# Kernel optimization log

Hardware: AMD Instinct MI355X
Metric: run time of the kernel (lower is better)

## Reference

```python
import jax, jax.numpy as jnp
import numpy as np

B, N, F_IN, F_OUT = 4, 4096, 128, 128

def setup_inputs() -> dict:
    key = jax.random.key(0)
    k1, k2, k3 = jax.random.split(key, 3)
    x = jax.random.normal(k1, (B, N, F_IN), dtype=jnp.float32)
    adj = jax.random.uniform(k2, (B, N, N), dtype=jnp.float32)
    weight = jax.random.normal(k3, (F_IN, F_OUT), dtype=jnp.float32) * (6.0 / (F_IN + F_OUT)) ** 0.5
    bias = jnp.zeros((F_OUT,), dtype=jnp.float32)
    return {"x": x, "adj": adj, "weight": weight, "bias": bias}

def reference(x, adj, weight, bias):
    # Z = D^{-1/2} A D^{-1/2} X W + b   (activation=None)
    degree = jnp.sum(adj, axis=-1)                       # [B, N]
    d_inv = jnp.power(degree + 1e-6, -0.5)               # [B, N]
    # diag(d_inv) @ A @ diag(d_inv) == row/col elementwise scaling
    adj_norm = d_inv[:, :, None] * adj * d_inv[:, None, :]  # [B, N, N]
    z = jnp.einsum('bnm,bmf->bnf', adj_norm, x)          # [B, N, F_in]
    z = jnp.einsum('bnf,fo->bno', z, weight) + bias      # [B, N, F_out]
    return z
```

## Files before the change

### kernel.cpp

```cpp
#include <hip/hip_runtime.h>
#include <hip/hip_bf16.h>
#include <stdint.h>


#define NROW 4096
#define FDIM 128
#define NBATCH 4

typedef __bf16 bf16x8 __attribute__((ext_vector_type(8)));
typedef float f32x4 __attribute__((ext_vector_type(4)));

__global__ __launch_bounds__(256) void k_degree(const float* __restrict__ adj,
                                                float* __restrict__ dinv) {
  const int row = blockIdx.x * 4 + (threadIdx.x >> 6);
  const int lane = threadIdx.x & 63;
  const float4* arow = (const float4*)(adj + (size_t)row * NROW);
  float s = 0.f;
#pragma unroll
  for (int i = 0; i < 16; ++i) {
    float4 v = arow[lane + i * 64];
    s += (v.x + v.y) + (v.z + v.w);
  }
#pragma unroll
  for (int off = 32; off > 0; off >>= 1) s += __shfl_down(s, off, 64);
  if (lane == 0) dinv[row] = 1.0f / sqrtf(s + 1e-6f);
}

__global__ __launch_bounds__(256) void k_xst(const float* __restrict__ x,
                                             const float* __restrict__ dinv,
                                             __hip_bfloat16* __restrict__ xst) {
  const int bid = blockIdx.x;
  const int b = bid >> 7;
  const int m0 = (bid & 127) * 32;
  const int tid = threadIdx.x;
  __shared__ float tile[32 * 132];

  {
    const int ml = tid >> 3;
    const int fl = (tid & 7) * 16;
    const float dv = dinv[b * NROW + m0 + ml];
    const float* gx = x + ((size_t)b * NROW + m0 + ml) * FDIM + fl;
    float* dst = &tile[ml * 132 + fl];
#pragma unroll
    for (int j = 0; j < 16; j += 4) {
      float4 v = *(const float4*)(gx + j);
      v.x *= dv; v.y *= dv; v.z *= dv; v.w *= dv;
      *(float4*)(dst + j) = v;
    }
  }
  __syncthreads();
  {
    const int f = tid >> 1;
    const int mc = (tid & 1) * 16;
    union { __hip_bfloat16 h[16]; uint4 v[2]; } tmp;
#pragma unroll
    for (int j = 0; j < 16; ++j)
      tmp.h[j] = __float2bfloat16(tile[(mc + j) * 132 + f]);
    __hip_bfloat16* dst = xst + ((size_t)b * FDIM + f) * NROW + m0 + mc;
    *(uint4*)(dst) = tmp.v[0];
    *(uint4*)(dst + 8) = tmp.v[1];
  }
}

#define MT 32
#define KC 64
#define AS_ST 72
#define BS_ST 72
#define ZS_ST 136

__global__ __launch_bounds__(256, 2)
void k_gemm(const float* __restrict__ adj, const __hip_bfloat16* __restrict__ xst,
            const float* __restrict__ dinv, const float* __restrict__ w,
            const float* __restrict__ bias, float* __restrict__ out) {
  __shared__ union {
    struct { __hip_bfloat16 As[2][MT * AS_ST]; __hip_bfloat16 Bs[2][FDIM * BS_ST]; } lp;
    __hip_bfloat16 Zs[MT * ZS_ST];
  } sm;
  __shared__ float dinv_s[MT];

  const int bid = blockIdx.x;
  const int xcd = bid & 7;
  const int b = xcd >> 1;
  const int mtile = (bid >> 3) * 2 + (xcd & 1);
  const int row0 = mtile * MT;

  const int tid = threadIdx.x;
  const int lane = tid & 63;
  const int wid = tid >> 6;
  const int l16 = lane & 15;
  const int quad = lane >> 4;

  if (tid < MT) dinv_s[tid] = dinv[b * NROW + row0 + tid];

  const float* adj_b = adj + ((size_t)b * NROW + row0) * NROW;
  const __hip_bfloat16* xst_b = xst + (size_t)b * FDIM * NROW;

  f32x4 zero4;
  zero4.x = 0.f; zero4.y = 0.f; zero4.z = 0.f; zero4.w = 0.f;
  f32x4 acc[2][2];
#pragma unroll
  for (int rt = 0; rt < 2; ++rt)
#pragma unroll
    for (int ct = 0; ct < 2; ++ct) acc[rt][ct] = zero4;

  const int ar = tid >> 3;
  const int ac = (tid & 7) * 8;
  const int bfr = tid >> 1;
  const int bcc = (tid & 1) * 32;
  const float* ga = adj_b + (size_t)ar * NROW + ac;
  const __hip_bfloat16* gb = xst_b + (size_t)bfr * NROW + bcc;

  float4 pa0 = *(const float4*)(ga);
  float4 pa1 = *(const float4*)(ga + 4);
  uint4 pb0 = ((const uint4*)gb)[0];
  uint4 pb1 = ((const uint4*)gb)[1];
  uint4 pb2 = ((const uint4*)gb)[2];
  uint4 pb3 = ((const uint4*)gb)[3];

  int p = 0;
  for (int k0 = 0; k0 < NROW; k0 += KC) {
    {
      union { __hip_bfloat16 h[8]; uint4 u; } t;
      t.h[0] = __float2bfloat16(pa0.x); t.h[1] = __float2bfloat16(pa0.y);
      t.h[2] = __float2bfloat16(pa0.z); t.h[3] = __float2bfloat16(pa0.w);
      t.h[4] = __float2bfloat16(pa1.x); t.h[5] = __float2bfloat16(pa1.y);
      t.h[6] = __float2bfloat16(pa1.z); t.h[7] = __float2bfloat16(pa1.w);
      *(uint4*)&sm.lp.As[p][ar * AS_ST + ac] = t.u;
      __hip_bfloat16* q = &sm.lp.Bs[p][bfr * BS_ST + bcc];
      *(uint4*)(q) = pb0;
      *(uint4*)(q + 8) = pb1;
      *(uint4*)(q + 16) = pb2;
      *(uint4*)(q + 24) = pb3;
    }
    if (k0 + KC < NROW) {
      const float* gan = ga + k0 + KC;
      pa0 = *(const float4*)(gan);
      pa1 = *(const float4*)(gan + 4);
      const __hip_bfloat16* gbn = gb + k0 + KC;
      pb0 = ((const uint4*)gbn)[0];
      pb1 = ((const uint4*)gbn)[1];
      pb2 = ((const uint4*)gbn)[2];
      pb3 = ((const uint4*)gbn)[3];
    }
    __syncthreads();
#pragma unroll
    for (int kk = 0; kk < 2; ++kk) {
      bf16x8 af[2], bfv[2];
#pragma unroll
      for (int rt = 0; rt < 2; ++rt)
        af[rt] = *(const bf16x8*)&sm.lp.As[p][(rt * 16 + l16) * AS_ST + kk * 32 + quad * 8];
#pragma unroll
      for (int ct = 0; ct < 2; ++ct)
        bfv[ct] = *(const bf16x8*)&sm.lp.Bs[p][(wid * 32 + ct * 16 + l16) * BS_ST + kk * 32 + quad * 8];
#pragma unroll
      for (int rt = 0; rt < 2; ++rt)
#pragma unroll
        for (int ct = 0; ct < 2; ++ct)
          acc[rt][ct] = __builtin_amdgcn_mfma_f32_16x16x32_bf16(af[rt], bfv[ct], acc[rt][ct], 0, 0, 0);
    }
    p ^= 1;
  }
  __syncthreads();

#pragma unroll
  for (int rt = 0; rt < 2; ++rt)
#pragma unroll
    for (int ct = 0; ct < 2; ++ct)
#pragma unroll
      for (int i = 0; i < 4; ++i) {
        int r = rt * 16 + quad * 4 + i;
        int c = wid * 32 + ct * 16 + l16;
        sm.Zs[r * ZS_ST + c] = __float2bfloat16(acc[rt][ct][i] * dinv_s[r]);
      }
  __syncthreads();

  f32x4 acc2[2][2];
#pragma unroll
  for (int rt = 0; rt < 2; ++rt)
#pragma unroll
    for (int ct = 0; ct < 2; ++ct) acc2[rt][ct] = zero4;
#pragma unroll
  for (int kk = 0; kk < 4; ++kk) {
    bf16x8 za[2], wb[2];
#pragma unroll
    for (int rt = 0; rt < 2; ++rt)
      za[rt] = *(const bf16x8*)&sm.Zs[(rt * 16 + l16) * ZS_ST + kk * 32 + quad * 8];
#pragma unroll
    for (int ct = 0; ct < 2; ++ct) {
      const int o = wid * 32 + ct * 16 + l16;
      const float* gw = w + (kk * 32 + quad * 8) * FDIM + o;
      union { __hip_bfloat16 h[8]; bf16x8 v; } tw;
#pragma unroll
      for (int j = 0; j < 8; ++j)
        tw.h[j] = __float2bfloat16(gw[j * FDIM]);
      wb[ct] = tw.v;
    }
#pragma unroll
    for (int rt = 0; rt < 2; ++rt)
#pragma unroll
      for (int ct = 0; ct < 2; ++ct)
        acc2[rt][ct] = __builtin_amdgcn_mfma_f32_16x16x32_bf16(za[rt], wb[ct], acc2[rt][ct], 0, 0, 0);
  }

  float bv[2];
  bv[0] = bias[wid * 32 + l16];
  bv[1] = bias[wid * 32 + 16 + l16];
  float* ob = out + ((size_t)b * NROW + row0) * FDIM;
#pragma unroll
  for (int rt = 0; rt < 2; ++rt)
#pragma unroll
    for (int ct = 0; ct < 2; ++ct)
#pragma unroll
      for (int i = 0; i < 4; ++i) {
        int r = rt * 16 + quad * 4 + i;
        int o = wid * 32 + ct * 16 + l16;
        ob[(size_t)r * FDIM + o] = acc2[rt][ct][i] + bv[ct];
      }
}

extern "C" void kernel_launch(void* const* d_in, const int* in_sizes, int n_in,
                              void* d_out, int out_size, void* d_ws, size_t ws_size,
                              hipStream_t stream) {
  const float* x    = (const float*)d_in[0];
  const float* adj  = (const float*)d_in[1];
  const float* w    = (const float*)d_in[2];
  const float* bias = (const float*)d_in[3];
  float* out = (float*)d_out;

  float* dinv = (float*)d_ws;
  __hip_bfloat16* xst =
      (__hip_bfloat16*)((char*)d_ws + (size_t)NBATCH * NROW * sizeof(float));

  k_degree<<<NBATCH * NROW / 4, 256, 0, stream>>>(adj, dinv);
  k_xst<<<512, 256, 0, stream>>>(x, dinv, xst);
  k_gemm<<<512, 256, 0, stream>>>(adj, xst, dinv, w, bias, out);
}
```

Baseline: 418.8 us.

## Pre-convert adjacency to bf16 during degree pass and pre-transpose weights

The degree kernel now also writes a bf16 copy of the adjacency matrix, so the main GEMM loads half as many bytes per tile and skips the per-iteration fp32-to-bf16 conversions. The weight matrix is transposed and converted to bf16 once by an extra block in the x-scaling kernel, which turns the strided fp32 weight gathers in the epilogue into vector loads. The cost is writing and re-reading a 128 MB bf16 workspace copy, so total memory traffic stays roughly the same. This path runs only when the workspace is large enough; otherwise the old fp32 path is used.

New measurement: 449.2 us. 1.07x slower.

```diff
diff --git a/kernel.cpp b/kernel.cpp
--- a/kernel.cpp
+++ b/kernel.cpp
@@ -9,6 +9,30 @@
 
 typedef __bf16 bf16x8 __attribute__((ext_vector_type(8)));
 typedef float f32x4 __attribute__((ext_vector_type(4)));
+
+__global__ __launch_bounds__(256) void k_degree_cvt(const float* __restrict__ adj,
+                                                    float* __restrict__ dinv,
+                                                    __hip_bfloat16* __restrict__ adjh) {
+  const int row = blockIdx.x * 4 + (threadIdx.x >> 6);
+  const int lane = threadIdx.x & 63;
+  const float4* arow = (const float4*)(adj + (size_t)row * NROW);
+  ushort4* hrow = (ushort4*)(adjh + (size_t)row * NROW);
+  float s = 0.f;
+#pragma unroll
+  for (int i = 0; i < 16; ++i) {
+    float4 v = arow[lane + i * 64];
+    s += (v.x + v.y) + (v.z + v.w);
+    union { __hip_bfloat16 h[4]; ushort4 u; } t;
+    t.h[0] = __float2bfloat16(v.x);
+    t.h[1] = __float2bfloat16(v.y);
+    t.h[2] = __float2bfloat16(v.z);
+    t.h[3] = __float2bfloat16(v.w);
+    hrow[lane + i * 64] = t.u;
+  }
+#pragma unroll
+  for (int off = 32; off > 0; off >>= 1) s += __shfl_down(s, off, 64);
+  if (lane == 0) dinv[row] = 1.0f / sqrtf(s + 1e-6f);
+}
 
 __global__ __launch_bounds__(256) void k_degree(const float* __restrict__ adj,
                                                 float* __restrict__ dinv) {
@@ -28,13 +52,28 @@
 
 __global__ __launch_bounds__(256) void k_xst(const float* __restrict__ x,
                                              const float* __restrict__ dinv,
-                                             __hip_bfloat16* __restrict__ xst) {
+                                             __hip_bfloat16* __restrict__ xst,
+                                             const float* __restrict__ w,
+                                             __hip_bfloat16* __restrict__ wt) {
   const int bid = blockIdx.x;
+  const int tid = threadIdx.x;
+
+  if (bid == 512) {
+    const int o = tid >> 1;
+    const int f0 = (tid & 1) * 64;
+    union { __hip_bfloat16 h[64]; uint4 v[8]; } t;
+#pragma unroll
+    for (int j = 0; j < 64; ++j)
+      t.h[j] = __float2bfloat16(w[(size_t)(f0 + j) * FDIM + o]);
+    uint4* dst = (uint4*)(wt + (size_t)o * FDIM + f0);
+#pragma unroll
+    for (int j = 0; j < 8; ++j) dst[j] = t.v[j];
+    return;
+  }
+
   const int b = bid >> 7;
   const int m0 = (bid & 127) * 32;
-  const int tid = threadIdx.x;
   __shared__ float tile[32 * 132];
-
   {
     const int ml = tid >> 3;
     const int fl = (tid & 7) * 16;
@@ -69,9 +108,146 @@
 #define ZS_ST 136
 
 __global__ __launch_bounds__(256, 2)
-void k_gemm(const float* __restrict__ adj, const __hip_bfloat16* __restrict__ xst,
-            const float* __restrict__ dinv, const float* __restrict__ w,
-            const float* __restrict__ bias, float* __restrict__ out) {
+void k_gemm_h(const __hip_bfloat16* __restrict__ adjh, const __hip_bfloat16* __restrict__ xst,
+              const float* __restrict__ dinv, const __hip_bfloat16* __restrict__ wt,
+              const float* __restrict__ bias, float* __restrict__ out) {
+  __shared__ union {
+    struct { __hip_bfloat16 As[2][MT * AS_ST]; __hip_bfloat16 Bs[2][FDIM * BS_ST]; } lp;
+    __hip_bfloat16 Zs[MT * ZS_ST];
+  } sm;
+  __shared__ float dinv_s[MT];
+
+  const int bid = blockIdx.x;
+  const int xcd = bid & 7;
+  const int b = xcd >> 1;
+  const int mtile = (bid >> 3) * 2 + (xcd & 1);
+  const int row0 = mtile * MT;
+
+  const int tid = threadIdx.x;
+  const int lane = tid & 63;
+  const int wid = tid >> 6;
+  const int l16 = lane & 15;
+  const int quad = lane >> 4;
+
+  if (tid < MT) dinv_s[tid] = dinv[b * NROW + row0 + tid];
+
+  const __hip_bfloat16* adjh_b = adjh + ((size_t)b * NROW + row0) * NROW;
+  const __hip_bfloat16* xst_b = xst + (size_t)b * FDIM * NROW;
+
+  f32x4 zero4;
+  zero4.x = 0.f; zero4.y = 0.f; zero4.z = 0.f; zero4.w = 0.f;
+  f32x4 acc[2][2];
+#pragma unroll
+  for (int rt = 0; rt < 2; ++rt)
+#pragma unroll
+    for (int ct = 0; ct < 2; ++ct) acc[rt][ct] = zero4;
+
+  const int ar = tid >> 3;
+  const int ac = (tid & 7) * 8;
+  const int bfr = tid >> 1;
+  const int bcc = (tid & 1) * 32;
+  const __hip_bfloat16* ga = adjh_b + (size_t)ar * NROW + ac;
+  const __hip_bfloat16* gb = xst_b + (size_t)bfr * NROW + bcc;
+
+  uint4 pa = *(const uint4*)(ga);
+  uint4 pb0 = ((const uint4*)gb)[0];
+  uint4 pb1 = ((const uint4*)gb)[1];
+  uint4 pb2 = ((const uint4*)gb)[2];
+  uint4 pb3 = ((const uint4*)gb)[3];
+
+  int p = 0;
+  for (int k0 = 0; k0 < NROW; k0 += KC) {
+    {
+      *(uint4*)&sm.lp.As[p][ar * AS_ST + ac] = pa;
+      __hip_bfloat16* q = &sm.lp.Bs[p][bfr * BS_ST + bcc];
+      *(uint4*)(q) = pb0;
+      *(uint4*)(q + 8) = pb1;
+      *(uint4*)(q + 16) = pb2;
+      *(uint4*)(q + 24) = pb3;
+    }
+    if (k0 + KC < NROW) {
+      pa = *(const uint4*)(ga + k0 + KC);
+      const __hip_bfloat16* gbn = gb + k0 + KC;
+      pb0 = ((const uint4*)gbn)[0];
+      pb1 = ((const uint4*)gbn)[1];
+      pb2 = ((const uint4*)gbn)[2];
+      pb3 = ((const uint4*)gbn)[3];
+    }
+    __syncthreads();
+#pragma unroll
+    for (int kk = 0; kk < 2; ++kk) {
+      bf16x8 af[2], bfv[2];
+#pragma unroll
+      for (int rt = 0; rt < 2; ++rt)
+        af[rt] = *(const bf16x8*)&sm.lp.As[p][(rt * 16 + l16) * AS_ST + kk * 32 + quad * 8];
+#pragma unroll
+      for (int ct = 0; ct < 2; ++ct)
+        bfv[ct] = *(const bf16x8*)&sm.lp.Bs[p][(wid * 32 + ct * 16 + l16) * BS_ST + kk * 32 + quad * 8];
+#pragma unroll
+      for (int rt = 0; rt < 2; ++rt)
+#pragma unroll
+        for (int ct = 0; ct < 2; ++ct)
+          acc[rt][ct] = __builtin_amdgcn_mfma_f32_16x16x32_bf16(af[rt], bfv[ct], acc[rt][ct], 0, 0, 0);
+    }
+    p ^= 1;
+  }
+  __syncthreads();
+
+#pragma unroll
+  for (int rt = 0; rt < 2; ++rt)
+#pragma unroll
+    for (int ct = 0; ct < 2; ++ct)
+#pragma unroll
+      for (int i = 0; i < 4; ++i) {
+        int r = rt * 16 + quad * 4 + i;
+        int c = wid * 32 + ct * 16 + l16;
+        sm.Zs[r * ZS_ST + c] = __float2bfloat16(acc[rt][ct][i] * dinv_s[r]);
+      }
+  __syncthreads();
+
+  f32x4 acc2[2][2];
+#pragma unroll
+  for (int rt = 0; rt < 2; ++rt)
+#pragma unroll
+    for (int ct = 0; ct < 2; ++ct) acc2[rt][ct] = zero4;
+#pragma unroll
+  for (int kk = 0; kk < 4; ++kk) {
+    bf16x8 za[2], wb[2];
+#pragma unroll
+    for (int rt = 0; rt < 2; ++rt)
+      za[rt] = *(const bf16x8*)&sm.Zs[(rt * 16 + l16) * ZS_ST + kk * 32 + quad * 8];
+#pragma unroll
+    for (int ct = 0; ct < 2; ++ct) {
+      const int o = wid * 32 + ct * 16 + l16;
+      wb[ct] = *(const bf16x8*)&wt[(size_t)o * FDIM + kk * 32 + quad * 8];
+    }
+#pragma unroll
+    for (int rt = 0; rt < 2; ++rt)
+#pragma unroll
+      for (int ct = 0; ct < 2; ++ct)
+        acc2[rt][ct] = __builtin_amdgcn_mfma_f32_16x16x32_bf16(za[rt], wb[ct], acc2[rt][ct], 0, 0, 0);
+  }
+
+  float bv[2];
+  bv[0] = bias[wid * 32 + l16];
+  bv[1] = bias[wid * 32 + 16 + l16];
+  float* ob = out + ((size_t)b * NROW + row0) * FDIM;
+#pragma unroll
+  for (int rt = 0; rt < 2; ++rt)
+#pragma unroll
+    for (int ct = 0; ct < 2; ++ct)
+#pragma unroll
+      for (int i = 0; i < 4; ++i) {
+        int r = rt * 16 + quad * 4 + i;
+        int o = wid * 32 + ct * 16 + l16;
+        ob[(size_t)r * FDIM + o] = acc2[rt][ct][i] + bv[ct];
+      }
+}
+
+__global__ __launch_bounds__(256, 2)
+void k_gemm_f32(const float* __restrict__ adj, const __hip_bfloat16* __restrict__ xst,
+                const float* __restrict__ dinv, const float* __restrict__ w,
+                const float* __restrict__ bias, float* __restrict__ out) {
   __shared__ union {
     struct { __hip_bfloat16 As[2][MT * AS_ST]; __hip_bfloat16 Bs[2][FDIM * BS_ST]; } lp;
     __hip_bfloat16 Zs[MT * ZS_ST];
@@ -227,11 +403,24 @@
   const float* bias = (const float*)d_in[3];
   float* out = (float*)d_out;
 
-  float* dinv = (float*)d_ws;
-  __hip_bfloat16* xst =
-      (__hip_bfloat16*)((char*)d_ws + (size_t)NBATCH * NROW * sizeof(float));
-
-  k_degree<<<NBATCH * NROW / 4, 256, 0, stream>>>(adj, dinv);
-  k_xst<<<512, 256, 0, stream>>>(x, dinv, xst);
-  k_gemm<<<512, 256, 0, stream>>>(adj, xst, dinv, w, bias, out);
-}
+  const size_t OFF_DINV = 0;
+  const size_t OFF_XST  = 65536;
+  const size_t OFF_WT   = OFF_XST + 4194304;
+  const size_t OFF_ADJH = OFF_WT + 32768;
+  const size_t NEED = OFF_ADJH + (size_t)NBATCH * NROW * NROW * 2;
+
+  float* dinv = (float*)((char*)d_ws + OFF_DINV);
+  __hip_bfloat16* xst  = (__hip_bfloat16*)((char*)d_ws + OFF_XST);
+  __hip_bfloat16* wt   = (__hip_bfloat16*)((char*)d_ws + OFF_WT);
+  __hip_bfloat16* adjh = (__hip_bfloat16*)((char*)d_ws + OFF_ADJH);
+
+  if (ws_size >= NEED) {
+    k_degree_cvt<<<NBATCH * NROW / 4, 256, 0, stream>>>(adj, dinv, adjh);
+    k_xst<<<513, 256, 0, stream>>>(x, dinv, xst, w, wt);
+    k_gemm_h<<<512, 256, 0, stream>>>(adjh, xst, dinv, wt, bias, out);
+  } else {
+    k_degree<<<NBATCH * NROW / 4, 256, 0, stream>>>(adj, dinv);
+    k_xst<<<512, 256, 0, stream>>>(x, dinv, xst, w, (__hip_bfloat16*)0);
+    k_gemm_f32<<<512, 256, 0, stream>>>(adj, xst, dinv, w, bias, out);
+  }
+}
```

## Prefetch two adjacency K-chunks ahead and pre-transpose weight to bf16

Applied to the files above, without the earlier changes.

The main GEMM loop is unrolled by two, with register prefetch sets for the A and B halves. This keeps two K-chunks of global loads in flight instead of one, to hide more memory latency on the adjacency stream. Separately, an extra block in the transpose kernel writes a bf16 transposed copy of W into workspace. The epilogue can then load weight fragments as one vector read instead of eight strided fp32 loads plus conversions. The cost is higher register pressure from the doubled prefetch buffers.

New measurement: 429.2 us. 1.02x slower.

```diff
diff --git a/kernel.cpp b/kernel.cpp
--- a/kernel.cpp
+++ b/kernel.cpp
@@ -28,13 +28,28 @@
 
 __global__ __launch_bounds__(256) void k_xst(const float* __restrict__ x,
                                              const float* __restrict__ dinv,
-                                             __hip_bfloat16* __restrict__ xst) {
+                                             __hip_bfloat16* __restrict__ xst,
+                                             const float* __restrict__ w,
+                                             __hip_bfloat16* __restrict__ wt) {
   const int bid = blockIdx.x;
+  const int tid = threadIdx.x;
+
+  if (bid == 512) {
+    const int o = tid >> 1;
+    const int f0 = (tid & 1) * 64;
+    union { __hip_bfloat16 h[64]; uint4 v[8]; } t;
+#pragma unroll
+    for (int j = 0; j < 64; ++j)
+      t.h[j] = __float2bfloat16(w[(size_t)(f0 + j) * FDIM + o]);
+    uint4* dst = (uint4*)(wt + (size_t)o * FDIM + f0);
+#pragma unroll
+    for (int j = 0; j < 8; ++j) dst[j] = t.v[j];
+    return;
+  }
+
   const int b = bid >> 7;
   const int m0 = (bid & 127) * 32;
-  const int tid = threadIdx.x;
   __shared__ float tile[32 * 132];
-
   {
     const int ml = tid >> 3;
     const int fl = (tid & 7) * 16;
@@ -70,7 +85,7 @@
 
 __global__ __launch_bounds__(256, 2)
 void k_gemm(const float* __restrict__ adj, const __hip_bfloat16* __restrict__ xst,
-            const float* __restrict__ dinv, const float* __restrict__ w,
+            const float* __restrict__ dinv, const __hip_bfloat16* __restrict__ wt,
             const float* __restrict__ bias, float* __restrict__ out) {
   __shared__ union {
     struct { __hip_bfloat16 As[2][MT * AS_ST]; __hip_bfloat16 Bs[2][FDIM * BS_ST]; } lp;
@@ -110,37 +125,42 @@
   const float* ga = adj_b + (size_t)ar * NROW + ac;
   const __hip_bfloat16* gb = xst_b + (size_t)bfr * NROW + bcc;
 
-  float4 pa0 = *(const float4*)(ga);
-  float4 pa1 = *(const float4*)(ga + 4);
-  uint4 pb0 = ((const uint4*)gb)[0];
-  uint4 pb1 = ((const uint4*)gb)[1];
-  uint4 pb2 = ((const uint4*)gb)[2];
-  uint4 pb3 = ((const uint4*)gb)[3];
-
-  int p = 0;
-  for (int k0 = 0; k0 < NROW; k0 += KC) {
+  float4 paA0 = *(const float4*)(ga);
+  float4 paA1 = *(const float4*)(ga + 4);
+  uint4 pbA0 = ((const uint4*)(gb))[0];
+  uint4 pbA1 = ((const uint4*)(gb))[1];
+  uint4 pbA2 = ((const uint4*)(gb))[2];
+  uint4 pbA3 = ((const uint4*)(gb))[3];
+  float4 paB0 = *(const float4*)(ga + KC);
+  float4 paB1 = *(const float4*)(ga + KC + 4);
+  uint4 pbB0 = ((const uint4*)(gb + KC))[0];
+  uint4 pbB1 = ((const uint4*)(gb + KC))[1];
+  uint4 pbB2 = ((const uint4*)(gb + KC))[2];
+  uint4 pbB3 = ((const uint4*)(gb + KC))[3];
+
+  for (int k0 = 0; k0 < NROW; k0 += 2 * KC) {
     {
       union { __hip_bfloat16 h[8]; uint4 u; } t;
-      t.h[0] = __float2bfloat16(pa0.x); t.h[1] = __float2bfloat16(pa0.y);
-      t.h[2] = __float2bfloat16(pa0.z); t.h[3] = __float2bfloat16(pa0.w);
-      t.h[4] = __float2bfloat16(pa1.x); t.h[5] = __float2bfloat16(pa1.y);
-      t.h[6] = __float2bfloat16(pa1.z); t.h[7] = __float2bfloat16(pa1.w);
-      *(uint4*)&sm.lp.As[p][ar * AS_ST + ac] = t.u;
-      __hip_bfloat16* q = &sm.lp.Bs[p][bfr * BS_ST + bcc];
-      *(uint4*)(q) = pb0;
-      *(uint4*)(q + 8) = pb1;
-      *(uint4*)(q + 16) = pb2;
-      *(uint4*)(q + 24) = pb3;
-    }
-    if (k0 + KC < NROW) {
-      const float* gan = ga + k0 + KC;
-      pa0 = *(const float4*)(gan);
-      pa1 = *(const float4*)(gan + 4);
-      const __hip_bfloat16* gbn = gb + k0 + KC;
-      pb0 = ((const uint4*)gbn)[0];
-      pb1 = ((const uint4*)gbn)[1];
-      pb2 = ((const uint4*)gbn)[2];
-      pb3 = ((const uint4*)gbn)[3];
+      t.h[0] = __float2bfloat16(paA0.x); t.h[1] = __float2bfloat16(paA0.y);
+      t.h[2] = __float2bfloat16(paA0.z); t.h[3] = __float2bfloat16(paA0.w);
+      t.h[4] = __float2bfloat16(paA1.x); t.h[5] = __float2bfloat16(paA1.y);
+      t.h[6] = __float2bfloat16(paA1.z); t.h[7] = __float2bfloat16(paA1.w);
+      *(uint4*)&sm.lp.As[0][ar * AS_ST + ac] = t.u;
+      __hip_bfloat16* q = &sm.lp.Bs[0][bfr * BS_ST + bcc];
+      *(uint4*)(q) = pbA0;
+      *(uint4*)(q + 8) = pbA1;
+      *(uint4*)(q + 16) = pbA2;
+      *(uint4*)(q + 24) = pbA3;
+    }
+    if (k0 + 2 * KC < NROW) {
+      const float* gan = ga + k0 + 2 * KC;
+      paA0 = *(const float4*)(gan);
+      paA1 = *(const float4*)(gan + 4);
+      const __hip_bfloat16* gbn = gb + k0 + 2 * KC;
+      pbA0 = ((const uint4*)gbn)[0];
+      pbA1 = ((const uint4*)gbn)[1];
+      pbA2 = ((const uint4*)gbn)[2];
+      pbA3 = ((const uint4*)gbn)[3];
     }
     __syncthreads();
 #pragma unroll
@@ -148,17 +168,56 @@
       bf16x8 af[2], bfv[2];
 #pragma unroll
       for (int rt = 0; rt < 2; ++rt)
-        af[rt] = *(const bf16x8*)&sm.lp.As[p][(rt * 16 + l16) * AS_ST + kk * 32 + quad * 8];
+        af[rt] = *(const bf16x8*)&sm.lp.As[0][(rt * 16 + l16) * AS_ST + kk * 32 + quad * 8];
 #pragma unroll
       for (int ct = 0; ct < 2; ++ct)
-        bfv[ct] = *(const bf16x8*)&sm.lp.Bs[p][(wid * 32 + ct * 16 + l16) * BS_ST + kk * 32 + quad * 8];
+        bfv[ct] = *(const bf16x8*)&sm.lp.Bs[0][(wid * 32 + ct * 16 + l16) * BS_ST + kk * 32 + quad * 8];
 #pragma unroll
       for (int rt = 0; rt < 2; ++rt)
 #pragma unroll
         for (int ct = 0; ct < 2; ++ct)
           acc[rt][ct] = __builtin_amdgcn_mfma_f32_16x16x32_bf16(af[rt], bfv[ct], acc[rt][ct], 0, 0, 0);
     }
-    p ^= 1;
+
+    {
+      union { __hip_bfloat16 h[8]; uint4 u; } t;
+      t.h[0] = __float2bfloat16(paB0.x); t.h[1] = __float2bfloat16(paB0.y);
+      t.h[2] = __float2bfloat16(paB0.z); t.h[3] = __float2bfloat16(paB0.w);
+      t.h[4] = __float2bfloat16(paB1.x); t.h[5] = __float2bfloat16(paB1.y);
+      t.h[6] = __float2bfloat16(paB1.z); t.h[7] = __float2bfloat16(paB1.w);
+      *(uint4*)&sm.lp.As[1][ar * AS_ST + ac] = t.u;
+      __hip_bfloat16* q = &sm.lp.Bs[1][bfr * BS_ST + bcc];
+      *(uint4*)(q) = pbB0;
+      *(uint4*)(q + 8) = pbB1;
+      *(uint4*)(q + 16) = pbB2;
+      *(uint4*)(q + 24) = pbB3;
+    }
+    if (k0 + 3 * KC < NROW) {
+      const float* gan = ga + k0 + 3 * KC;
+      paB0 = *(const float4*)(gan);
+      paB1 = *(const float4*)(gan + 4);
+      const __hip_bfloat16* gbn = gb + k0 + 3 * KC;
+      pbB0 = ((const uint4*)gbn)[0];
+      pbB1 = ((const uint4*)gbn)[1];
+      pbB2 = ((const uint4*)gbn)[2];
+      pbB3 = ((const uint4*)gbn)[3];
+    }
+    __syncthreads();
+#pragma unroll
+    for (int kk = 0; kk < 2; ++kk) {
+      bf16x8 af[2], bfv[2];
+#pragma unroll
+      for (int rt = 0; rt < 2; ++rt)
+        af[rt] = *(const bf16x8*)&sm.lp.As[1][(rt * 16 + l16) * AS_ST + kk * 32 + quad * 8];
+#pragma unroll
+      for (int ct = 0; ct < 2; ++ct)
+        bfv[ct] = *(const bf16x8*)&sm.lp.Bs[1][(wid * 32 + ct * 16 + l16) * BS_ST + kk * 32 + quad * 8];
+#pragma unroll
+      for (int rt = 0; rt < 2; ++rt)
+#pragma unroll
+        for (int ct = 0; ct < 2; ++ct)
+          acc[rt][ct] = __builtin_amdgcn_mfma_f32_16x16x32_bf16(af[rt], bfv[ct], acc[rt][ct], 0, 0, 0);
+    }
   }
   __syncthreads();
 
@@ -188,12 +247,7 @@
 #pragma unroll
     for (int ct = 0; ct < 2; ++ct) {
       const int o = wid * 32 + ct * 16 + l16;
-      const float* gw = w + (kk * 32 + quad * 8) * FDIM + o;
-      union { __hip_bfloat16 h[8]; bf16x8 v; } tw;
-#pragma unroll
-      for (int j = 0; j < 8; ++j)
-        tw.h[j] = __float2bfloat16(gw[j * FDIM]);
-      wb[ct] = tw.v;
+      wb[ct] = *(const bf16x8*)&wt[(size_t)o * FDIM + kk * 32 + quad * 8];
     }
 #pragma unroll
     for (int rt = 0; rt < 2; ++rt)
@@ -230,8 +284,11 @@
   float* dinv = (float*)d_ws;
   __hip_bfloat16* xst =
       (__hip_bfloat16*)((char*)d_ws + (size_t)NBATCH * NROW * sizeof(float));
+  __hip_bfloat16* wt =
+      (__hip_bfloat16*)((char*)d_ws + (size_t)NBATCH * NROW * sizeof(float)
+                        + (size_t)NBATCH * NROW * FDIM * sizeof(__hip_bfloat16));
 
   k_degree<<<NBATCH * NROW / 4, 256, 0, stream>>>(adj, dinv);
-  k_xst<<<512, 256, 0, stream>>>(x, dinv, xst);
-  k_gemm<<<512, 256, 0, stream>>>(adj, xst, dinv, w, bias, out);
-}
+  k_xst<<<513, 256, 0, stream>>>(x, dinv, xst, w, wt);
+  k_gemm<<<512, 256, 0, stream>>>(adj, xst, dinv, wt, bias, out);
+}
```

## Load X^T operand fragments directly from global and pretranspose weight to bf16

Applied to the files above, without the earlier changes.

In the main GEMM, the B operand (scaled, transposed X in bf16) is no longer staged through shared memory. Each wave loads its MFMA fragments straight from global memory into registers, with the next chunk prefetched between the two MFMA halves. This shrinks LDS use and removes the B-side shared-memory stores and reads. An extra block in the X-transpose kernel also builds a bf16 transposed copy of W, so the epilogue does vector loads instead of strided fp32 loads and per-element conversion. The trade-off is that the four waves in a block, and blocks on the same batch, now issue redundant global/L2 reads of X^T.

Result: slower. 443.7 us (+5.9%).

```diff
diff --git a/kernel.cpp b/kernel.cpp
--- a/kernel.cpp
+++ b/kernel.cpp
@@ -28,13 +28,28 @@
 
 __global__ __launch_bounds__(256) void k_xst(const float* __restrict__ x,
                                              const float* __restrict__ dinv,
-                                             __hip_bfloat16* __restrict__ xst) {
+                                             __hip_bfloat16* __restrict__ xst,
+                                             const float* __restrict__ w,
+                                             __hip_bfloat16* __restrict__ wt) {
   const int bid = blockIdx.x;
+  const int tid = threadIdx.x;
+
+  if (bid == 512) {
+    const int o = tid >> 1;
+    const int f0 = (tid & 1) * 64;
+    union { __hip_bfloat16 h[64]; uint4 v[8]; } t;
+#pragma unroll
+    for (int j = 0; j < 64; ++j)
+      t.h[j] = __float2bfloat16(w[(size_t)(f0 + j) * FDIM + o]);
+    uint4* dst = (uint4*)(wt + (size_t)o * FDIM + f0);
+#pragma unroll
+    for (int j = 0; j < 8; ++j) dst[j] = t.v[j];
+    return;
+  }
+
   const int b = bid >> 7;
   const int m0 = (bid & 127) * 32;
-  const int tid = threadIdx.x;
   __shared__ float tile[32 * 132];
-
   {
     const int ml = tid >> 3;
     const int fl = (tid & 7) * 16;
@@ -65,15 +80,14 @@
 #define MT 32
 #define KC 64
 #define AS_ST 72
-#define BS_ST 72
 #define ZS_ST 136
 
 __global__ __launch_bounds__(256, 2)
 void k_gemm(const float* __restrict__ adj, const __hip_bfloat16* __restrict__ xst,
-            const float* __restrict__ dinv, const float* __restrict__ w,
+            const float* __restrict__ dinv, const __hip_bfloat16* __restrict__ wt,
             const float* __restrict__ bias, float* __restrict__ out) {
   __shared__ union {
-    struct { __hip_bfloat16 As[2][MT * AS_ST]; __hip_bfloat16 Bs[2][FDIM * BS_ST]; } lp;
+    __hip_bfloat16 As[2][MT * AS_ST];
     __hip_bfloat16 Zs[MT * ZS_ST];
   } sm;
   __shared__ float dinv_s[MT];
@@ -95,6 +109,9 @@
   const float* adj_b = adj + ((size_t)b * NROW + row0) * NROW;
   const __hip_bfloat16* xst_b = xst + (size_t)b * FDIM * NROW;
 
+  const __hip_bfloat16* gb0 = xst_b + (size_t)(wid * 32 + l16) * NROW + quad * 8;
+  const __hip_bfloat16* gb1 = gb0 + (size_t)16 * NROW;
+
   f32x4 zero4;
   zero4.x = 0.f; zero4.y = 0.f; zero4.z = 0.f; zero4.w = 0.f;
   f32x4 acc[2][2];
@@ -105,58 +122,53 @@
 
   const int ar = tid >> 3;
   const int ac = (tid & 7) * 8;
-  const int bfr = tid >> 1;
-  const int bcc = (tid & 1) * 32;
   const float* ga = adj_b + (size_t)ar * NROW + ac;
-  const __hip_bfloat16* gb = xst_b + (size_t)bfr * NROW + bcc;
 
   float4 pa0 = *(const float4*)(ga);
   float4 pa1 = *(const float4*)(ga + 4);
-  uint4 pb0 = ((const uint4*)gb)[0];
-  uint4 pb1 = ((const uint4*)gb)[1];
-  uint4 pb2 = ((const uint4*)gb)[2];
-  uint4 pb3 = ((const uint4*)gb)[3];
+  bf16x8 pbf00 = *(const bf16x8*)(gb0);
+  bf16x8 pbf01 = *(const bf16x8*)(gb1);
+  bf16x8 pbf10 = *(const bf16x8*)(gb0 + 32);
+  bf16x8 pbf11 = *(const bf16x8*)(gb1 + 32);
 
   int p = 0;
   for (int k0 = 0; k0 < NROW; k0 += KC) {
+    const int kn = k0 + KC;
     {
       union { __hip_bfloat16 h[8]; uint4 u; } t;
       t.h[0] = __float2bfloat16(pa0.x); t.h[1] = __float2bfloat16(pa0.y);
       t.h[2] = __float2bfloat16(pa0.z); t.h[3] = __float2bfloat16(pa0.w);
       t.h[4] = __float2bfloat16(pa1.x); t.h[5] = __float2bfloat16(pa1.y);
       t.h[6] = __float2bfloat16(pa1.z); t.h[7] = __float2bfloat16(pa1.w);
-      *(uint4*)&sm.lp.As[p][ar * AS_ST + ac] = t.u;
-      __hip_bfloat16* q = &sm.lp.Bs[p][bfr * BS_ST + bcc];
-      *(uint4*)(q) = pb0;
-      *(uint4*)(q + 8) = pb1;
-      *(uint4*)(q + 16) = pb2;
-      *(uint4*)(q + 24) = pb3;
-    }
-    if (k0 + KC < NROW) {
-      const float* gan = ga + k0 + KC;
+      *(uint4*)&sm.As[p][ar * AS_ST + ac] = t.u;
+    }
+    if (kn < NROW) {
+      const float* gan = ga + kn;
       pa0 = *(const float4*)(gan);
       pa1 = *(const float4*)(gan + 4);
-      const __hip_bfloat16* gbn = gb + k0 + KC;
-      pb0 = ((const uint4*)gbn)[0];
-      pb1 = ((const uint4*)gbn)[1];
-      pb2 = ((const uint4*)gbn)[2];
-      pb3 = ((const uint4*)gbn)[3];
     }
     __syncthreads();
-#pragma unroll
-    for (int kk = 0; kk < 2; ++kk) {
-      bf16x8 af[2], bfv[2];
-#pragma unroll
-      for (int rt = 0; rt < 2; ++rt)
-        af[rt] = *(const bf16x8*)&sm.lp.As[p][(rt * 16 + l16) * AS_ST + kk * 32 + quad * 8];
-#pragma unroll
-      for (int ct = 0; ct < 2; ++ct)
-        bfv[ct] = *(const bf16x8*)&sm.lp.Bs[p][(wid * 32 + ct * 16 + l16) * BS_ST + kk * 32 + quad * 8];
-#pragma unroll
-      for (int rt = 0; rt < 2; ++rt)
-#pragma unroll
-        for (int ct = 0; ct < 2; ++ct)
-          acc[rt][ct] = __builtin_amdgcn_mfma_f32_16x16x32_bf16(af[rt], bfv[ct], acc[rt][ct], 0, 0, 0);
+
+    bf16x8 af00 = *(const bf16x8*)&sm.As[p][(l16) * AS_ST + quad * 8];
+    bf16x8 af01 = *(const bf16x8*)&sm.As[p][(16 + l16) * AS_ST + quad * 8];
+    acc[0][0] = __builtin_amdgcn_mfma_f32_16x16x32_bf16(af00, pbf00, acc[0][0], 0, 0, 0);
+    acc[0][1] = __builtin_amdgcn_mfma_f32_16x16x32_bf16(af00, pbf01, acc[0][1], 0, 0, 0);
+    acc[1][0] = __builtin_amdgcn_mfma_f32_16x16x32_bf16(af01, pbf00, acc[1][0], 0, 0, 0);
+    acc[1][1] = __builtin_amdgcn_mfma_f32_16x16x32_bf16(af01, pbf01, acc[1][1], 0, 0, 0);
+    if (kn < NROW) {
+      pbf00 = *(const bf16x8*)(gb0 + kn);
+      pbf01 = *(const bf16x8*)(gb1 + kn);
+    }
+
+    bf16x8 af10 = *(const bf16x8*)&sm.As[p][(l16) * AS_ST + 32 + quad * 8];
+    bf16x8 af11 = *(const bf16x8*)&sm.As[p][(16 + l16) * AS_ST + 32 + quad * 8];
+    acc[0][0] = __builtin_amdgcn_mfma_f32_16x16x32_bf16(af10, pbf10, acc[0][0], 0, 0, 0);
+    acc[0][1] = __builtin_amdgcn_mfma_f32_16x16x32_bf16(af10, pbf11, acc[0][1], 0, 0, 0);
+    acc[1][0] = __builtin_amdgcn_mfma_f32_16x16x32_bf16(af11, pbf10, acc[1][0], 0, 0, 0);
+    acc[1][1] = __builtin_amdgcn_mfma_f32_16x16x32_bf16(af11, pbf11, acc[1][1], 0, 0, 0);
+    if (kn < NROW) {
+      pbf10 = *(const bf16x8*)(gb0 + kn + 32);
+      pbf11 = *(const bf16x8*)(gb1 + kn + 32);
     }
     p ^= 1;
   }
@@ -188,12 +200,7 @@
 #pragma unroll
     for (int ct = 0; ct < 2; ++ct) {
       const int o = wid * 32 + ct * 16 + l16;
-      const float* gw = w + (kk * 32 + quad * 8) * FDIM + o;
-      union { __hip_bfloat16 h[8]; bf16x8 v; } tw;
-#pragma unroll
-      for (int j = 0; j < 8; ++j)
-        tw.h[j] = __float2bfloat16(gw[j * FDIM]);
-      wb[ct] = tw.v;
+      wb[ct] = *(const bf16x8*)&wt[(size_t)o * FDIM + kk * 32 + quad * 8];
     }
 #pragma unroll
     for (int rt = 0; rt < 2; ++rt)
@@ -230,8 +237,11 @@
   float* dinv = (float*)d_ws;
   __hip_bfloat16* xst =
       (__hip_bfloat16*)((char*)d_ws + (size_t)NBATCH * NROW * sizeof(float));
+  __hip_bfloat16* wt =
+      (__hip_bfloat16*)((char*)d_ws + (size_t)NBATCH * NROW * sizeof(float)
+                        + (size_t)NBATCH * NROW * FDIM * sizeof(__hip_bfloat16));
 
   k_degree<<<NBATCH * NROW / 4, 256, 0, stream>>>(adj, dinv);
-  k_xst<<<512, 256, 0, stream>>>(x, dinv, xst);
-  k_gemm<<<512, 256, 0, stream>>>(adj, xst, dinv, w, bias, out);
-}
+  k_xst<<<513, 256, 0, stream>>>(x, dinv, xst, w, wt);
+  k_gemm<<<512, 256, 0, stream>>>(adj, xst, dinv, wt, bias, out);
+}
```
